# Optimization experiments

Measured on AMD Instinct MI355X. Metric: run time of the kernel, lower is better.

## Reference

```python
import jax, jax.numpy as jnp
import numpy as np

B, S, EMBED, FFN, NQ = 8, 2048, 1024, 4096, 8

def setup_inputs() -> dict:
    key = jax.random.key(0)
    ks = jax.random.split(key, 6)
    return {
        "x": jax.random.normal(ks[0], (B, S, EMBED), dtype=jnp.float32),
        "theta": jax.random.normal(ks[1], (NQ,), dtype=jnp.float32),
        "W1": jax.random.normal(ks[2], (FFN, NQ), dtype=jnp.float32) * (1.0 / np.sqrt(NQ)),
        "b1": jax.random.normal(ks[3], (FFN,), dtype=jnp.float32) * 0.02,
        "W2": jax.random.normal(ks[4], (EMBED, FFN), dtype=jnp.float32) * (1.0 / np.sqrt(FFN)),
        "b2": jax.random.normal(ks[5], (EMBED,), dtype=jnp.float32) * 0.02,
    }

def reference(x, theta, W1, b1, W2, b2):
    # Quantum layer (product circuit, closed form): per qubit i,
    # |0> -RX(x_i)-> -RY(theta_i)->, <PauliZ> = cos(x_i) * cos(theta_i).
    nq = theta.shape[0]
    q = jnp.cos(x[..., :nq]) * jnp.cos(theta)        # [B,S,NQ]
    # dropout is identity in eval mode
    h = jax.nn.relu(jnp.einsum('bsq,fq->bsf', q, W1) + b1)  # [B,S,FFN]
    return jnp.einsum('bsf,ef->bse', h, W2) + b2            # [B,S,EMBED]
```

## Files before the change

kernel.cpp:

```cpp
#include <hip/hip_runtime.h>
#include <cstdint>
#include <cstddef>

#define AS1 __attribute__((address_space(1)))
#define AS3 __attribute__((address_space(3)))

typedef __bf16 bf16x8 __attribute__((ext_vector_type(8)));
typedef float  f32x4  __attribute__((ext_vector_type(4)));

#define MDIM 16384
#define NDIM 1024
#define KDIM 4096
#define NQ   8

#define BM 128
#define BN 128
#define BK 64

__global__ __launch_bounds__(256) void conv_w2_kernel(const float* __restrict__ W2,
                                                      __bf16* __restrict__ W2b) {
    size_t base = ((size_t)blockIdx.x * 256 + threadIdx.x) * 8;
    float4 a = *(const float4*)(W2 + base);
    float4 b = *(const float4*)(W2 + base + 4);
    bf16x8 v;
    v[0] = (__bf16)a.x; v[1] = (__bf16)a.y; v[2] = (__bf16)a.z; v[3] = (__bf16)a.w;
    v[4] = (__bf16)b.x; v[5] = (__bf16)b.y; v[6] = (__bf16)b.z; v[7] = (__bf16)b.w;
    *(bf16x8*)(W2b + base) = v;
}

#define QROWS 32
__global__ __launch_bounds__(256) void qh_kernel(const float* __restrict__ x,
                                                 const float* __restrict__ theta,
                                                 const float* __restrict__ W1,
                                                 const float* __restrict__ b1,
                                                 __bf16* __restrict__ H) {
    __shared__ __align__(16) float qs[QROWS][NQ];
    const int t  = threadIdx.x;
    const int r0 = blockIdx.x * QROWS;

    {
        const int qr = t >> 3, qi = t & 7;
        const float xv = x[(size_t)(r0 + qr) * 1024 + qi];
        qs[qr][qi] = __cosf(xv) * __cosf(theta[qi]);
    }
    __syncthreads();

#pragma unroll
    for (int fc = 0; fc < 2; ++fc) {
        const int f0 = fc * 2048 + t * 8;
        float w[8][8];
#pragma unroll
        for (int fr = 0; fr < 8; ++fr) {
            float4 a = *(const float4*)(W1 + (size_t)(f0 + fr) * NQ);
            float4 b = *(const float4*)(W1 + (size_t)(f0 + fr) * NQ + 4);
            w[fr][0] = a.x; w[fr][1] = a.y; w[fr][2] = a.z; w[fr][3] = a.w;
            w[fr][4] = b.x; w[fr][5] = b.y; w[fr][6] = b.z; w[fr][7] = b.w;
        }
        float bias[8];
        {
            float4 a = *(const float4*)(b1 + f0);
            float4 b = *(const float4*)(b1 + f0 + 4);
            bias[0] = a.x; bias[1] = a.y; bias[2] = a.z; bias[3] = a.w;
            bias[4] = b.x; bias[5] = b.y; bias[6] = b.z; bias[7] = b.w;
        }
#pragma unroll 1
        for (int r = 0; r < QROWS; ++r) {
            const float4 qa = *(const float4*)&qs[r][0];
            const float4 qb = *(const float4*)&qs[r][4];
            float q[8] = { qa.x, qa.y, qa.z, qa.w, qb.x, qb.y, qb.z, qb.w };
            bf16x8 o;
#pragma unroll
            for (int fr = 0; fr < 8; ++fr) {
                float a = bias[fr];
#pragma unroll
                for (int i = 0; i < 8; ++i) a += q[i] * w[fr][i];
                o[fr] = (__bf16)fmaxf(a, 0.f);
            }
            *(bf16x8*)(H + (size_t)(r0 + r) * KDIM + f0) = o;
        }
    }
}

__global__ __launch_bounds__(256, 3) void gemm_bt_kernel(const __bf16* __restrict__ A,
                                                         const __bf16* __restrict__ B,
                                                         const float* __restrict__ bias,
                                                         float* __restrict__ C) {
    __shared__ __align__(16) __bf16 Al[BM * BK];
    __shared__ __align__(16) __bf16 Bl[BN * BK];

    const int tid  = threadIdx.x;
    const int wave = tid >> 6;
    const int lane = tid & 63;
    const int id   = blockIdx.x;
    const int xcd  = id & 7;
    const int s    = id >> 3;
    const int bn   = s & 7;
    const int bm   = xcd * 16 + (s >> 3);

    const int lr = lane >> 3;
    const int ul = (lane & 7) ^ lr;
    const __bf16* gA0 = A + (size_t)(bm * BM + wave * 32 + lr) * KDIM + ul * 8;
    const __bf16* gB0 = B + (size_t)(bn * BN + wave * 32 + lr) * KDIM + ul * 8;
    __bf16* lA0 = &Al[(wave * 32) * BK];
    __bf16* lB0 = &Bl[(wave * 32) * BK];

    const int ml = lane & 15;
    const int kq = lane >> 4;
    const int sw = lane & 7;
    const int wm = (wave & 1) * 64;
    const int wn = (wave >> 1) * 64;

    f32x4 acc[4][4] = {};

    for (int kt = 0; kt < KDIM; kt += BK) {
        __syncthreads();
#pragma unroll
        for (int c = 0; c < 4; ++c) {
            __builtin_amdgcn_global_load_lds((AS1 void*)(gA0 + (size_t)c * 8 * KDIM + kt),
                                             (AS3 void*)(lA0 + c * 8 * BK), 16, 0, 0);
            __builtin_amdgcn_global_load_lds((AS1 void*)(gB0 + (size_t)c * 8 * KDIM + kt),
                                             (AS3 void*)(lB0 + c * 8 * BK), 16, 0, 0);
        }
        __syncthreads();
#pragma unroll
        for (int st = 0; st < 2; ++st) {
            const int u = ((st * 4 + kq) ^ sw) * 8;
            bf16x8 afrag[4], bfrag[4];
#pragma unroll
            for (int i = 0; i < 4; ++i) {
                afrag[i] = *(const bf16x8*)&Al[(wm + i * 16 + ml) * BK + u];
                bfrag[i] = *(const bf16x8*)&Bl[(wn + i * 16 + ml) * BK + u];
            }
#pragma unroll
            for (int i = 0; i < 4; ++i)
#pragma unroll
                for (int j = 0; j < 4; ++j)
                    acc[i][j] = __builtin_amdgcn_mfma_f32_16x16x32_bf16(afrag[i], bfrag[j], acc[i][j], 0, 0, 0);
        }
    }

    const int cm0 = bm * BM + wm;
    const int cn0 = bn * BN + wn;
#pragma unroll
    for (int j = 0; j < 4; ++j) {
        const int col = cn0 + j * 16 + ml;
        const float bv = bias[col];
#pragma unroll
        for (int i = 0; i < 4; ++i) {
            const int row0 = cm0 + i * 16 + kq * 4;
#pragma unroll
            for (int r = 0; r < 4; ++r)
                C[(size_t)(row0 + r) * NDIM + col] = acc[i][j][r] + bv;
        }
    }
}

extern "C" void kernel_launch(void* const* d_in, const int* in_sizes, int n_in,
                              void* d_out, int out_size, void* d_ws, size_t ws_size,
                              hipStream_t stream) {
    const float* x     = (const float*)d_in[0];
    const float* theta = (const float*)d_in[1];
    const float* W1    = (const float*)d_in[2];
    const float* b1    = (const float*)d_in[3];
    const float* W2    = (const float*)d_in[4];
    const float* b2    = (const float*)d_in[5];
    float* out = (float*)d_out;

    __bf16* H   = (__bf16*)d_ws;
    __bf16* W2b = (__bf16*)((char*)d_ws + (size_t)MDIM * KDIM * 2);

    conv_w2_kernel<<<(KDIM * NDIM) / (256 * 8), 256, 0, stream>>>(W2, W2b);
    qh_kernel<<<MDIM / QROWS, 256, 0, stream>>>(x, theta, W1, b1, H);
    gemm_bt_kernel<<<(MDIM / BM) * (NDIM / BN), 256, 0, stream>>>(H, W2b, b2, out);
}
```

Baseline: 279.8 us.

## Rewrite GEMM with 256x256 tiles, 8 waves, and double-buffered LDS pipeline

Replaces the 128x128 single-buffered GEMM with a 256x256 tile computed by 512 threads (8 waves, each owning a 128x64 output slab). LDS is double-buffered in 32-wide K slices so global-to-LDS loads for the next tile are issued inside each compute phase. Explicit barriers, waitcnt and setprio are used to overlap them with MFMA work. This aims to raise arithmetic intensity and hide memory latency, at the cost of 128KB of LDS, more accumulator registers, and a fragile hand-scheduled synchronisation scheme.

```diff
diff --git a/kernel.cpp b/kernel.cpp
--- a/kernel.cpp
+++ b/kernel.cpp
@@ -12,10 +12,6 @@
 #define NDIM 1024
 #define KDIM 4096
 #define NQ   8
-
-#define BM 128
-#define BN 128
-#define BK 64
 
 __global__ __launch_bounds__(256) void conv_w2_kernel(const float* __restrict__ W2,
                                                       __bf16* __restrict__ W2b) {
@@ -81,72 +77,106 @@
     }
 }
 
-__global__ __launch_bounds__(256, 3) void gemm_bt_kernel(const __bf16* __restrict__ A,
+#define BM 256
+#define BN 256
+#define BK 64
+#define SLICE 8192
+
+__device__ __forceinline__ void stage_slice(const __bf16* gsrc, __bf16* ldst) {
+    __builtin_amdgcn_global_load_lds((AS1 void*)gsrc, (AS3 void*)ldst, 16, 0, 0);
+    __builtin_amdgcn_global_load_lds((AS1 void*)(gsrc + (size_t)128 * KDIM),
+                                     (AS3 void*)(ldst + 4096), 16, 0, 0);
+}
+
+template<int KS, int MG, bool VM>
+__device__ __forceinline__ void phase(const __bf16* bufR, f32x4 (&acc)[8][4],
+                                      int axo, int bxo,
+                                      const __bf16* gsrc, __bf16* ldst) {
+    const __bf16* As = bufR + KS * SLICE;
+    const __bf16* Bs = bufR + (2 + KS) * SLICE;
+    bf16x8 af[4], bfr[4];
+#pragma unroll
+    for (int i = 0; i < 4; ++i)
+        af[i] = *(const bf16x8*)(As + axo + MG * 2048 + i * 512);
+#pragma unroll
+    for (int j = 0; j < 4; ++j)
+        bfr[j] = *(const bf16x8*)(Bs + bxo + j * 512);
+    stage_slice(gsrc, ldst);
+    __builtin_amdgcn_s_barrier();
+    asm volatile("s_waitcnt lgkmcnt(0)" ::: "memory");
+    __builtin_amdgcn_sched_barrier(0);
+    __builtin_amdgcn_s_setprio(1);
+#pragma unroll
+    for (int i = 0; i < 4; ++i)
+#pragma unroll
+        for (int j = 0; j < 4; ++j)
+            acc[MG * 4 + i][j] = __builtin_amdgcn_mfma_f32_16x16x32_bf16(
+                af[i], bfr[j], acc[MG * 4 + i][j], 0, 0, 0);
+    __builtin_amdgcn_s_setprio(0);
+    if constexpr (VM)
+        asm volatile("s_waitcnt vmcnt(4)" ::: "memory");
+    __builtin_amdgcn_s_barrier();
+}
+
+__global__ __launch_bounds__(512, 2) void gemm_bt_kernel(const __bf16* __restrict__ A,
                                                          const __bf16* __restrict__ B,
                                                          const float* __restrict__ bias,
                                                          float* __restrict__ C) {
-    __shared__ __align__(16) __bf16 Al[BM * BK];
-    __shared__ __align__(16) __bf16 Bl[BN * BK];
-
-    const int tid  = threadIdx.x;
-    const int wave = tid >> 6;
-    const int lane = tid & 63;
-    const int id   = blockIdx.x;
-    const int xcd  = id & 7;
-    const int s    = id >> 3;
-    const int bn   = s & 7;
-    const int bm   = xcd * 16 + (s >> 3);
-
-    const int lr = lane >> 3;
-    const int ul = (lane & 7) ^ lr;
-    const __bf16* gA0 = A + (size_t)(bm * BM + wave * 32 + lr) * KDIM + ul * 8;
-    const __bf16* gB0 = B + (size_t)(bn * BN + wave * 32 + lr) * KDIM + ul * 8;
-    __bf16* lA0 = &Al[(wave * 32) * BK];
-    __bf16* lB0 = &Bl[(wave * 32) * BK];
-
-    const int ml = lane & 15;
-    const int kq = lane >> 4;
-    const int sw = lane & 7;
-    const int wm = (wave & 1) * 64;
-    const int wn = (wave >> 1) * 64;
-
-    f32x4 acc[4][4] = {};
-
-    for (int kt = 0; kt < KDIM; kt += BK) {
-        __syncthreads();
-#pragma unroll
-        for (int c = 0; c < 4; ++c) {
-            __builtin_amdgcn_global_load_lds((AS1 void*)(gA0 + (size_t)c * 8 * KDIM + kt),
-                                             (AS3 void*)(lA0 + c * 8 * BK), 16, 0, 0);
-            __builtin_amdgcn_global_load_lds((AS1 void*)(gB0 + (size_t)c * 8 * KDIM + kt),
-                                             (AS3 void*)(lB0 + c * 8 * BK), 16, 0, 0);
-        }
-        __syncthreads();
-#pragma unroll
-        for (int st = 0; st < 2; ++st) {
-            const int u = ((st * 4 + kq) ^ sw) * 8;
-            bf16x8 afrag[4], bfrag[4];
-#pragma unroll
-            for (int i = 0; i < 4; ++i) {
-                afrag[i] = *(const bf16x8*)&Al[(wm + i * 16 + ml) * BK + u];
-                bfrag[i] = *(const bf16x8*)&Bl[(wn + i * 16 + ml) * BK + u];
-            }
-#pragma unroll
-            for (int i = 0; i < 4; ++i)
-#pragma unroll
-                for (int j = 0; j < 4; ++j)
-                    acc[i][j] = __builtin_amdgcn_mfma_f32_16x16x32_bf16(afrag[i], bfrag[j], acc[i][j], 0, 0, 0);
-        }
-    }
-
-    const int cm0 = bm * BM + wm;
-    const int cn0 = bn * BN + wn;
+    __shared__ __align__(16) __bf16 lds[2 * 4 * SLICE];
+
+    const int tid = threadIdx.x;
+    const int w   = tid >> 6;
+    const int l   = tid & 63;
+    const int id  = blockIdx.x;
+    const int xcd = id & 7;
+    const int s   = id >> 3;
+    const int bn  = s & 3;
+    const int bm  = xcd * 8 + (s >> 2);
+
+    const int wm = w >> 2;
+    const int wn = w & 3;
+
+    const int lr  = l >> 2;
+    const int ucl = (l & 3) ^ (lr & 3);
+    const __bf16* gA0 = A + (size_t)(bm * BM + w * 16 + lr) * KDIM + ucl * 8;
+    const __bf16* gB0 = B + (size_t)(bn * BN + w * 16 + lr) * KDIM + ucl * 8;
+    const int w512 = w * 512;
+
+    const int ml  = l & 15;
+    const int kq  = l >> 4;
+    const int fo  = (kq ^ (ml & 3)) << 3;
+    const int axo = (wm * 128 + ml) * 32 + fo;
+    const int bxo = (wn * 64 + ml) * 32 + fo;
+
+    f32x4 acc[8][4] = {};
+
+    stage_slice(gA0,      lds + 0 * SLICE + w512);
+    stage_slice(gB0,      lds + 2 * SLICE + w512);
+    stage_slice(gA0 + 32, lds + 1 * SLICE + w512);
+    stage_slice(gB0 + 32, lds + 3 * SLICE + w512);
+    asm volatile("s_waitcnt vmcnt(4)" ::: "memory");
+    __builtin_amdgcn_s_barrier();
+
+#pragma unroll 1
+    for (int t = 0; t < KDIM / BK; ++t) {
+        const __bf16* bufR = lds + (t & 1) * (4 * SLICE);
+        __bf16* bufW = lds + ((t + 1) & 1) * (4 * SLICE);
+        const int tn = (t < KDIM / BK - 1) ? (t + 1) * BK : (KDIM / BK - 1) * BK;
+
+        phase<0, 0, false>(bufR, acc, axo, bxo, gA0 + tn,      bufW + 0 * SLICE + w512);
+        phase<0, 1, true >(bufR, acc, axo, bxo, gB0 + tn,      bufW + 2 * SLICE + w512);
+        phase<1, 0, false>(bufR, acc, axo, bxo, gA0 + tn + 32, bufW + 1 * SLICE + w512);
+        phase<1, 1, true >(bufR, acc, axo, bxo, gB0 + tn + 32, bufW + 3 * SLICE + w512);
+    }
+
+    const int cm0 = bm * BM + wm * 128;
+    const int cn0 = bn * BN + wn * 64;
 #pragma unroll
     for (int j = 0; j < 4; ++j) {
         const int col = cn0 + j * 16 + ml;
         const float bv = bias[col];
 #pragma unroll
-        for (int i = 0; i < 4; ++i) {
+        for (int i = 0; i < 8; ++i) {
             const int row0 = cm0 + i * 16 + kq * 4;
 #pragma unroll
             for (int r = 0; r < 4; ++r)
@@ -171,5 +201,5 @@
 
     conv_w2_kernel<<<(KDIM * NDIM) / (256 * 8), 256, 0, stream>>>(W2, W2b);
     qh_kernel<<<MDIM / QROWS, 256, 0, stream>>>(x, theta, W1, b1, H);
-    gemm_bt_kernel<<<(MDIM / BM) * (NDIM / BN), 256, 0, stream>>>(H, W2b, b2, out);
-}
+    gemm_bt_kernel<<<(MDIM / BM) * (NDIM / BN), 512, 0, stream>>>(H, W2b, b2, out);
+}
```

Measured after the change: 281.0 us. Within noise of the previous version (+0.5%).
